# Performance work log

Measured on AMD Instinct MI355X. Metric: run time of the kernel, lower is better.

The kernel has to match this reference:

```python
import jax, jax.numpy as jnp
import numpy as np

N_DIS = 25000   # disease nodes: indices [0, 25000)
N_MIR = 25000   # mirna nodes:  indices [25000, 50000)
N = N_DIS + N_MIR
E = 600000
EMB = 128
HID = 128


def setup_inputs() -> dict:
    key = jax.random.key(0)
    ks = jax.random.split(key, 14)
    d_features = jax.random.normal(ks[0], (N_DIS, 383), jnp.float32)
    m_features = jax.random.normal(ks[1], (N_MIR, 495), jnp.float32)
    src = jax.random.randint(ks[2], (E,), 0, N, jnp.int32)
    dst = jax.random.randint(ks[3], (E,), 0, N, jnp.int32)
    def lin(k, fan_in, fan_out):
        lim = 1.0 / np.sqrt(fan_in)
        return jax.random.uniform(k, (fan_in, fan_out), jnp.float32, -lim, lim)
    return {
        "d_features": d_features,
        "m_features": m_features,
        "src": src,
        "dst": dst,
        "W_d": lin(ks[4], 383, EMB), "b_d": jnp.zeros((EMB,), jnp.float32),
        "W_m": lin(ks[5], 495, EMB), "b_m": jnp.zeros((EMB,), jnp.float32),
        "W_self1": lin(ks[6], EMB, HID), "W_neigh1": lin(ks[7], EMB, HID),
        "b1": jnp.zeros((HID,), jnp.float32),
        "W_self2": lin(ks[8], HID, HID), "W_neigh2": lin(ks[9], HID, HID),
        "b2": jnp.zeros((HID,), jnp.float32),
    }


def reference(d_features, m_features, src, dst,
              W_d, b_d, W_m, b_m,
              W_self1, W_neigh1, b1, W_self2, W_neigh2, b2):
    # Per-type embedding projection (torch.no_grad in original; dropout eval=identity)
    h_d = d_features @ W_d + b_d            # [N_DIS, EMB]
    h_m = m_features @ W_m + b_m            # [N_MIR, EMB]
    h = jnp.concatenate([h_d, h_m], axis=0)  # [N, EMB]

    # in-degree for mean aggregation (isolated nodes -> mean 0, like DGL fn.mean)
    deg = jax.ops.segment_sum(jnp.ones(src.shape, h.dtype), dst, num_segments=N)
    inv_deg = 1.0 / jnp.maximum(deg, 1.0)    # [N]

    def sage(x, W_self, W_neigh, b):
        # gather src feats, segment-mean into dst, then combine (DGL SAGEConv 'mean')
        agg = jax.ops.segment_sum(x[src], dst, num_segments=N) * inv_deg[:, None]
        return x @ W_self + agg @ W_neigh + b

    h = jax.nn.relu(sage(h, W_self1, W_neigh1, b1))
    h = sage(h, W_self2, W_neigh2, b2)
    return h
```

## Files before the change

### kernel.cpp

```cpp
#include <hip/hip_runtime.h>

#define N_DIS 25000
#define N_MIR 25000
#define NN    50000
#define E_NUM 600000
#define EMB   128

typedef __attribute__((ext_vector_type(8))) short short8v;
typedef __attribute__((ext_vector_type(4))) float floatx4;

typedef const unsigned int __attribute__((address_space(1))) as1_u32;
typedef unsigned int __attribute__((address_space(3))) as3_u32;

__device__ __forceinline__ void gld16(const void* g, void* lds) {
    __builtin_amdgcn_global_load_lds((as1_u32*)g, (as3_u32*)lds, 16, 0, 0);
}

__device__ __forceinline__ floatx4 mfma_bf16_16x16x32(short8v a, short8v b, floatx4 c) {
    asm("v_mfma_f32_16x16x32_bf16 %0, %1, %2, %0" : "+v"(c) : "v"(a), "v"(b));
    return c;
}

__device__ __forceinline__ float us2f(unsigned short u) {
    return __uint_as_float(((unsigned)u) << 16);
}
__device__ __forceinline__ unsigned short f2us(float f) {
    unsigned u = __float_as_uint(f);
    unsigned r = ((u >> 16) & 1u) + 0x7FFFu;
    u += r;
    return (unsigned short)(u >> 16);
}
__device__ __forceinline__ float loadf(const void* p, size_t i, bool isbf) {
    if (isbf) return us2f(((const unsigned short*)p)[i]);
    return ((const float*)p)[i];
}

__global__ __launch_bounds__(256) void gs_zero(int* counts, int* flags) {
    int i = blockIdx.x * blockDim.x + threadIdx.x;
    if (i < NN) counts[i] = 0;
    if (i < 8) flags[i] = 0;
}

__global__ __launch_bounds__(64) void gs_setflag(int* flags, int v) {
    if (threadIdx.x == 0) flags[0] = v;
}

__global__ __launch_bounds__(256) void gs_probe(const void* x, int* flags) {
    const unsigned* u = (const unsigned*)x;
    unsigned w = u[threadIdx.x];
    int e = (int)((w >> 7) & 0xFF);
    if (e >= 118 && e <= 135) atomicAdd(&flags[0], 1);
}

__global__ __launch_bounds__(256) void gs_prepw(const void* Wd, const void* Wm,
                                                const void* Ws1, const void* Wn1,
                                                const void* Ws2, const void* Wn2,
                                                const int* flags, unsigned short* wt) {
    const bool isbf = flags[0] > 128;
    const int t = threadIdx.x;
    const int w = blockIdx.x >> 2;
    const int cq = (blockIdx.x & 3) * 32;
    const void* W;
    unsigned short* oh;
    unsigned short* ol;
    int K, Kp;
    if (w == 0)      { W = Wd;  oh = wt + 0;      ol = wt + 49152;  K = 383; Kp = 384; }
    else if (w == 1) { W = Wm;  oh = wt + 98304;  ol = wt + 163840; K = 495; Kp = 512; }
    else if (w == 2) { W = Ws1; oh = wt + 229376; ol = wt + 245760; K = 128; Kp = 128; }
    else if (w == 3) { W = Wn1; oh = wt + 262144; ol = wt + 278528; K = 128; Kp = 128; }
    else if (w == 4) { W = Ws2; oh = wt + 294912; ol = wt + 311296; K = 128; Kp = 128; }
    else             { W = Wn2; oh = wt + 327680; ol = wt + 344064; K = 128; Kp = 128; }
    for (int c = cq; c < cq + 32; ++c) {
        for (int k = t; k < Kp; k += 256) {
            float x = (k < K) ? loadf(W, (size_t)k * EMB + c, isbf) : 0.f;
            unsigned short h = f2us(x);
            oh[(size_t)c * Kp + k] = h;
            ol[(size_t)c * Kp + k] = f2us(x - us2f(h));
        }
    }
}

__global__ __launch_bounds__(256) void gs_count(const int* dst, int* counts) {
    int e = blockIdx.x * blockDim.x + threadIdx.x;
    if (e < E_NUM) {
        unsigned d = (unsigned)dst[e];
        if (d < (unsigned)NN) atomicAdd(&counts[d], 1);
    }
}

__global__ __launch_bounds__(256) void gs_scan1(const int* counts, int* row_start, int* bsums) {
    __shared__ int tsum[256];
    const int t = threadIdx.x;
    const int base = blockIdx.x * 1024 + t * 4;
    int v0 = (base + 0 < NN) ? counts[base + 0] : 0;
    int v1 = (base + 1 < NN) ? counts[base + 1] : 0;
    int v2 = (base + 2 < NN) ? counts[base + 2] : 0;
    int v3 = (base + 3 < NN) ? counts[base + 3] : 0;
    int s = v0 + v1 + v2 + v3;
    tsum[t] = s;
    __syncthreads();
    for (int off = 1; off < 256; off <<= 1) {
        int xv = 0;
        if (t >= off) xv = tsum[t - off];
        __syncthreads();
        tsum[t] += xv;
        __syncthreads();
    }
    int excl = tsum[t] - s;
    if (base + 0 < NN) row_start[base + 0] = excl;
    excl += v0;
    if (base + 1 < NN) row_start[base + 1] = excl;
    excl += v1;
    if (base + 2 < NN) row_start[base + 2] = excl;
    excl += v2;
    if (base + 3 < NN) row_start[base + 3] = excl;
    if (t == 255) bsums[blockIdx.x] = tsum[255];
}

__global__ __launch_bounds__(64) void gs_scan2(int* bsums, int* row_start, int nb) {
    if (threadIdx.x == 0) {
        int run = 0;
        for (int i = 0; i < nb; ++i) {
            int v = bsums[i];
            bsums[i] = run;
            run += v;
        }
        row_start[NN] = run;
    }
}

__global__ __launch_bounds__(256) void gs_scan3(int* row_start, int* cursor, const int* bsums) {
    const int t = threadIdx.x;
    const int base = blockIdx.x * 1024 + t * 4;
    const int add = bsums[blockIdx.x];
    for (int i = 0; i < 4; ++i) {
        int idx = base + i;
        if (idx < NN) {
            int v = row_start[idx] + add;
            row_start[idx] = v;
            cursor[idx] = v;
        }
    }
}

__global__ __launch_bounds__(256) void gs_scatter(const int* src, const int* dst, int* cursor,
                                                  int* eidx) {
    int e = blockIdx.x * blockDim.x + threadIdx.x;
    if (e < E_NUM) {
        unsigned d = (unsigned)dst[e];
        unsigned sv = (unsigned)src[e];
        if (d < (unsigned)NN && sv < (unsigned)NN) {
            int p = atomicAdd(&cursor[d], 1);
            eidx[p] = (int)sv;
        }
    }
}

__global__ __launch_bounds__(256) void gs_aggp(const unsigned short* __restrict__ xh,
                                               const unsigned short* __restrict__ xl,
                                               const int* __restrict__ row_start,
                                               const int* __restrict__ eidx,
                                               unsigned short* __restrict__ oh,
                                               unsigned short* __restrict__ ol) {
    const int t = threadIdx.x;
    const int row = blockIdx.x * 8 + (t >> 5);
    const int c4 = (t & 31) * 4;
    if (row >= NN) return;
    const int s0 = row_start[row];
    const int s1 = row_start[row + 1];
    float a0 = 0.f, a1 = 0.f, a2 = 0.f, a3 = 0.f;
    float b0 = 0.f, b1 = 0.f, b2 = 0.f, b3 = 0.f;
    int e = s0;
    for (; e + 1 < s1; e += 2) {
        int sa = eidx[e];
        int sb = eidx[e + 1];
        ushort4 ha = *(const ushort4*)&xh[(size_t)sa * EMB + c4];
        ushort4 la = *(const ushort4*)&xl[(size_t)sa * EMB + c4];
        ushort4 hb = *(const ushort4*)&xh[(size_t)sb * EMB + c4];
        ushort4 lb = *(const ushort4*)&xl[(size_t)sb * EMB + c4];
        a0 += us2f(ha.x) + us2f(la.x); a1 += us2f(ha.y) + us2f(la.y);
        a2 += us2f(ha.z) + us2f(la.z); a3 += us2f(ha.w) + us2f(la.w);
        b0 += us2f(hb.x) + us2f(lb.x); b1 += us2f(hb.y) + us2f(lb.y);
        b2 += us2f(hb.z) + us2f(lb.z); b3 += us2f(hb.w) + us2f(lb.w);
    }
    if (e < s1) {
        int sa = eidx[e];
        ushort4 ha = *(const ushort4*)&xh[(size_t)sa * EMB + c4];
        ushort4 la = *(const ushort4*)&xl[(size_t)sa * EMB + c4];
        a0 += us2f(ha.x) + us2f(la.x); a1 += us2f(ha.y) + us2f(la.y);
        a2 += us2f(ha.z) + us2f(la.z); a3 += us2f(ha.w) + us2f(la.w);
    }
    float inv = (s1 > s0) ? 1.f / (float)(s1 - s0) : 0.f;
    float f0 = (a0 + b0) * inv, f1 = (a1 + b1) * inv;
    float f2 = (a2 + b2) * inv, f3 = (a3 + b3) * inv;
    ushort4 vh, vl;
    unsigned short h;
    h = f2us(f0); vh.x = h; vl.x = f2us(f0 - us2f(h));
    h = f2us(f1); vh.y = h; vl.y = f2us(f1 - us2f(h));
    h = f2us(f2); vh.z = h; vl.z = f2us(f2 - us2f(h));
    h = f2us(f3); vh.w = h; vl.w = f2us(f3 - us2f(h));
    *(ushort4*)&oh[(size_t)row * EMB + c4] = vh;
    *(ushort4*)&ol[(size_t)row * EMB + c4] = vl;
}

__global__ __launch_bounds__(256, 3) void gs_mmp(
    const void* __restrict__ Xa, int Ka, const unsigned short* __restrict__ WAh,
    const unsigned short* __restrict__ WAl, int KpA, const void* __restrict__ ba,
    const void* __restrict__ Xb, int Kb, const unsigned short* __restrict__ WBh,
    const unsigned short* __restrict__ WBl, int KpB, const void* __restrict__ bb,
    int splitB, int Ma, int Mb,
    const int* __restrict__ flags, unsigned short* __restrict__ outH,
    unsigned short* __restrict__ outL) {
    __shared__ __align__(16) unsigned char sm[49152];
    unsigned char* smXH = sm;
    unsigned char* smXL = sm + 8192;
    unsigned char* smWH = sm + 16384;
    unsigned char* smWL = sm + 32768;
    const bool isbf = flags[0] > 128;
    const int t = threadIdx.x;
    const bool sideB = (int)blockIdx.x >= splitB;
    const void* X1 = sideB ? Xb : Xa;
    const unsigned short* W1h = sideB ? WBh : WAh;
    const unsigned short* W1l = sideB ? WBl : WAl;
    const int K1 = sideB ? Kb : Ka;
    const int Kp1 = sideB ? KpB : KpA;
    const void* bias = sideB ? bb : ba;
    const int M = sideB ? Mb : Ma;
    const int r0 = (sideB ? ((int)blockIdx.x - splitB) : (int)blockIdx.x) * 64;
    unsigned short* oh = outH + (sideB ? (size_t)Ma * EMB : 0);
    unsigned short* ol = outL + (sideB ? (size_t)Ma * EMB : 0);

    const int l = t & 63;
    const int wv = t >> 6;
    const int wr = wv >> 1, wc = wv & 1;
    const int lr = l & 15, lg = l >> 4;

    floatx4 acc[2][4];
#pragma unroll
    for (int rt = 0; rt < 2; ++rt)
#pragma unroll
        for (int ct = 0; ct < 4; ++ct) acc[rt][ct] = (floatx4){0.f, 0.f, 0.f, 0.f};

    const int nch1 = (K1 + 63) >> 6;
    const int srX = t >> 2;
    const int skX = (t & 3) << 4;
    const bool xbf = isbf;

    for (int ch = 0; ch < nch1; ++ch) {
        const int ck0 = ch << 6;
        __syncthreads();
#pragma unroll
        for (int i = 0; i < 4; ++i) {
            const int p = (wv << 12) + (i << 10) + (l << 4);
            const int col = p >> 7;
            const int g16 = p & 0x7F;
            const size_t so = ((size_t)col * Kp1 + ck0) * 2 + (size_t)(g16 ^ ((col & 7) << 4));
            gld16((const unsigned char*)W1h + so, smWH + (wv << 12) + (i << 10));
            if (!isbf) gld16((const unsigned char*)W1l + so, smWL + (wv << 12) + (i << 10));
        }
        {
            const int gr = r0 + srX;
            unsigned xu[16];
#pragma unroll
            for (int j = 0; j < 16; ++j) {
                int gk = ck0 + skX + j;
                unsigned v = 0u;
                if (gr < M && gk < K1)
                    v = xbf ? (unsigned)((const unsigned short*)X1)[(size_t)gr * K1 + gk]
                            : ((const unsigned*)X1)[(size_t)gr * K1 + gk];
                xu[j] = v;
            }
            const int rowoff = srX << 7;
            const int swz = (srX & 7) << 4;
#pragma unroll
            for (int g = 0; g < 2; ++g) {
                short8v vh, vl;
#pragma unroll
                for (int e = 0; e < 8; ++e) {
                    unsigned u = xu[(g << 3) + e];
                    if (xbf) {
                        vh[e] = (short)u;
                        vl[e] = 0;
                    } else {
                        unsigned short h = (unsigned short)(u >> 16);
                        vh[e] = (short)h;
                        vl[e] = (short)f2us(__uint_as_float(u) - us2f(h));
                    }
                }
                const int off = rowoff + ((((skX << 1) + (g << 4))) ^ swz);
                *(short8v*)(smXH + off) = vh;
                if (!xbf) *(short8v*)(smXL + off) = vl;
            }
        }
        __syncthreads();
#pragma unroll
        for (int ks = 0; ks < 2; ++ks) {
            const int kbyte = (ks << 6) + (lg << 4);
            short8v ah[2], al[2];
#pragma unroll
            for (int rt = 0; rt < 2; ++rt) {
                const int row = wr * 32 + rt * 16 + lr;
                const int off = (row << 7) + (kbyte ^ ((row & 7) << 4));
                ah[rt] = *(const short8v*)(smXH + off);
                if (!xbf) al[rt] = *(const short8v*)(smXL + off);
            }
#pragma unroll
            for (int ct = 0; ct < 4; ++ct) {
                const int col = wc * 64 + ct * 16 + lr;
                const int boff = (col << 7) + (kbyte ^ ((col & 7) << 4));
                short8v bh = *(const short8v*)(smWH + boff);
                acc[0][ct] = mfma_bf16_16x16x32(ah[0], bh, acc[0][ct]);
                acc[1][ct] = mfma_bf16_16x16x32(ah[1], bh, acc[1][ct]);
                if (!xbf) {
                    acc[0][ct] = mfma_bf16_16x16x32(al[0], bh, acc[0][ct]);
                    acc[1][ct] = mfma_bf16_16x16x32(al[1], bh, acc[1][ct]);
                }
                if (!isbf) {
                    short8v bl = *(const short8v*)(smWL + boff);
                    acc[0][ct] = mfma_bf16_16x16x32(ah[0], bl, acc[0][ct]);
                    acc[1][ct] = mfma_bf16_16x16x32(ah[1], bl, acc[1][ct]);
                }
            }
        }
    }

#pragma unroll
    for (int ct = 0; ct < 4; ++ct) {
        const int col = wc * 64 + ct * 16 + lr;
        const float bbv = loadf(bias, col, isbf);
#pragma unroll
        for (int rt = 0; rt < 2; ++rt) {
#pragma unroll
            for (int rr = 0; rr < 4; ++rr) {
                const int row = r0 + wr * 32 + rt * 16 + (lg << 2) + rr;
                if (row < M) {
                    float v = acc[rt][ct][rr] + bbv;
                    unsigned short h = f2us(v);
                    oh[(size_t)row * EMB + col] = h;
                    ol[(size_t)row * EMB + col] = f2us(v - us2f(h));
                }
            }
        }
    }
}

__global__ __launch_bounds__(512, 4) void gs_mml(
    const unsigned short* __restrict__ X1h, const unsigned short* __restrict__ X1l,
    const unsigned short* __restrict__ W1h, const unsigned short* __restrict__ W1l,
    const unsigned short* __restrict__ X2h, const unsigned short* __restrict__ X2l,
    const unsigned short* __restrict__ W2h, const unsigned short* __restrict__ W2l,
    const void* __restrict__ bias, const int* __restrict__ flags,
    float* __restrict__ outf, unsigned short* __restrict__ outh,
    unsigned short* __restrict__ outl, int do_relu) {
    __shared__ __align__(16) unsigned char sm[65536];
    unsigned char* smXH = sm;
    unsigned char* smXL = sm + 16384;
    unsigned char* smWH = sm + 32768;
    unsigned char* smWL = sm + 49152;
    const bool isbf = flags[0] > 128;
    const int t = threadIdx.x;
    const int r0 = (int)blockIdx.x * 128;
    const int l = t & 63;
    const int wv = t >> 6;
    const int wr = wv >> 1, wc = wv & 1;
    const int lr = l & 15, lg = l >> 4;

    floatx4 acc[2][4];
#pragma unroll
    for (int rt = 0; rt < 2; ++rt)
#pragma unroll
        for (int ct = 0; ct < 4; ++ct) acc[rt][ct] = (floatx4){0.f, 0.f, 0.f, 0.f};

    const int plane = wv >> 1;

    for (int ch = 0; ch < 4; ++ch) {
        const unsigned short* xh = (ch < 2) ? X1h : X2h;
        const unsigned short* xl = (ch < 2) ? X1l : X2l;
        const unsigned short* wh = (ch < 2) ? W1h : W2h;
        const unsigned short* wl = (ch < 2) ? W1l : W2l;
        const int ck0b = (ch & 1) << 7;

        __syncthreads();
#pragma unroll
        for (int i = 0; i < 8; ++i) {
            const int q = ((wv & 1) << 13) + (i << 10) + (l << 4);
            const int rc = q >> 7;
            const int g16 = q & 0x7F;
            const int off = g16 ^ ((rc & 7) << 4);
            if (plane == 0) {
                const int gr = (r0 + rc < NN) ? (r0 + rc) : (NN - 1);
                gld16((const unsigned char*)xh + (size_t)gr * 256 + ck0b + off, smXH + q);
            } else if (plane == 1) {
                const int gr = (r0 + rc < NN) ? (r0 + rc) : (NN - 1);
                gld16((const unsigned char*)xl + (size_t)gr * 256 + ck0b + off, smXL + q);
            } else if (plane == 2) {
                gld16((const unsigned char*)wh + (size_t)rc * 256 + ck0b + off, smWH + q);
            } else if (!isbf) {
                gld16((const unsigned char*)wl + (size_t)rc * 256 + ck0b + off, smWL + q);
            }
        }
        __syncthreads();

#pragma unroll
        for (int ks = 0; ks < 2; ++ks) {
            const int kbyte = (ks << 6) + (lg << 4);
            short8v ah[2], al[2];
#pragma unroll
            for (int rt = 0; rt < 2; ++rt) {
                const int row = wr * 32 + rt * 16 + lr;
                const int off = (row << 7) + (kbyte ^ ((row & 7) << 4));
                ah[rt] = *(const short8v*)(smXH + off);
                al[rt] = *(const short8v*)(smXL + off);
            }
#pragma unroll
            for (int ct = 0; ct < 4; ++ct) {
                const int col = wc * 64 + ct * 16 + lr;
                const int boff = (col << 7) + (kbyte ^ ((col & 7) << 4));
                short8v bh = *(const short8v*)(smWH + boff);
                acc[0][ct] = mfma_bf16_16x16x32(ah[0], bh, acc[0][ct]);
                acc[1][ct] = mfma_bf16_16x16x32(ah[1], bh, acc[1][ct]);
                acc[0][ct] = mfma_bf16_16x16x32(al[0], bh, acc[0][ct]);
                acc[1][ct] = mfma_bf16_16x16x32(al[1], bh, acc[1][ct]);
                if (!isbf) {
                    short8v bl = *(const short8v*)(smWL + boff);
                    acc[0][ct] = mfma_bf16_16x16x32(ah[0], bl, acc[0][ct]);
                    acc[1][ct] = mfma_bf16_16x16x32(ah[1], bl, acc[1][ct]);
                }
            }
        }
    }

#pragma unroll
    for (int ct = 0; ct < 4; ++ct) {
        const int col = wc * 64 + ct * 16 + lr;
        const float bbv = loadf(bias, col, isbf);
#pragma unroll
        for (int rt = 0; rt < 2; ++rt) {
#pragma unroll
            for (int rr = 0; rr < 4; ++rr) {
                const int row = r0 + wr * 32 + rt * 16 + (lg << 2) + rr;
                if (row < NN) {
                    float v = acc[rt][ct][rr] + bbv;
                    if (do_relu) v = v > 0.f ? v : 0.f;
                    if (outf) {
                        outf[(size_t)row * EMB + col] = v;
                    } else {
                        unsigned short h = f2us(v);
                        outh[(size_t)row * EMB + col] = h;
                        outl[(size_t)row * EMB + col] = f2us(v - us2f(h));
                    }
                }
            }
        }
    }
}

extern "C" __attribute__((visibility("default"))) void kernel_launch(
    void* const* d_in, const int* in_sizes, int n_in, void* d_out, int out_size, void* d_ws,
    size_t ws_size, hipStream_t stream) {
    int iDF = 0, iMF = 1, iSRC = 2, iDST = 3, iWD = 4, iBD = 5, iWM = 6, iBM = 7;
    int iWS1 = 8, iWN1 = 9, iB1 = 10, iWS2 = 11, iWN2 = 12, iB2 = 13;
    long u0 = in_sizes ? (long)in_sizes[0] : 9575000L;
    int dt = -1;
    if (u0 == 49024L || u0 == 98048L || u0 == 196096L) {
        iWD = 0; iWM = 1; iWN1 = 2; iWN2 = 3; iWS1 = 4; iWS2 = 5;
        iB1 = 6; iB2 = 7; iBD = 8; iBM = 9; iDF = 10; iDST = 11; iMF = 12; iSRC = 13;
        if (u0 == 98048L) dt = 1;
        else if (u0 == 196096L) dt = 0;
    } else {
        if (u0 == 19150000L) dt = 1;
        else if (u0 == 38300000L) dt = 0;
    }
    const void* d_features = d_in[iDF];
    const void* m_features = d_in[iMF];
    const int* src = (const int*)d_in[iSRC];
    const int* dst = (const int*)d_in[iDST];
    const void* W_d = d_in[iWD];
    const void* b_d = d_in[iBD];
    const void* W_m = d_in[iWM];
    const void* b_m = d_in[iBM];
    const void* W_self1 = d_in[iWS1];
    const void* W_neigh1 = d_in[iWN1];
    const void* b1 = d_in[iB1];
    const void* W_self2 = d_in[iWS2];
    const void* W_neigh2 = d_in[iWN2];
    const void* b2v = d_in[iB2];

    char* w = (char*)d_ws;
    int* flags = (int*)(w + 0);
    int* counts = (int*)(w + 64);
    int* row_start = (int*)(w + 200064);
    int* cursor = (int*)(w + 400128);
    int* bsums = (int*)(w + 600128);
    int* eidx = (int*)(w + 600384);
    unsigned short* wt = (unsigned short*)(w + 3000448);
    unsigned short* wt_hd = wt + 0;
    unsigned short* wt_ld = wt + 49152;
    unsigned short* wt_hm = wt + 98304;
    unsigned short* wt_lm = wt + 163840;
    unsigned short* wt_hs1 = wt + 229376;
    unsigned short* wt_ls1 = wt + 245760;
    unsigned short* wt_hn1 = wt + 262144;
    unsigned short* wt_ln1 = wt + 278528;
    unsigned short* wt_hs2 = wt + 294912;
    unsigned short* wt_ls2 = wt + 311296;
    unsigned short* wt_hn2 = wt + 327680;
    unsigned short* wt_ln2 = wt + 344064;
    unsigned short* hFh = (unsigned short*)(w + 3721344);
    unsigned short* hFl = (unsigned short*)(w + 16521344);
    unsigned short* h1Fh = (unsigned short*)(w + 29321344);
    unsigned short* h1Fl = (unsigned short*)(w + 42121344);
    unsigned short* ag1h = (unsigned short*)d_out;
    unsigned short* ag1l = ag1h + 6400000;
    unsigned short* ag2h = hFh;
    unsigned short* ag2l = hFl;

    const int NB_SCAN = (NN + 1023) / 1024;
    const int EB = (E_NUM + 255) / 256;
    const int ZB = (NN + 255) / 256;

    hipLaunchKernelGGL(gs_zero, dim3(ZB), dim3(256), 0, stream, counts, flags);
    if (dt == 1)
        hipLaunchKernelGGL(gs_setflag, dim3(1), dim3(64), 0, stream, flags, 1000);
    else if (dt == 0)
        hipLaunchKernelGGL(gs_setflag, dim3(1), dim3(64), 0, stream, flags, 0);
    else
        hipLaunchKernelGGL(gs_probe, dim3(1), dim3(256), 0, stream, d_features, flags);

    hipLaunchKernelGGL(gs_prepw, dim3(24), dim3(256), 0, stream, W_d, W_m, W_self1, W_neigh1,
                       W_self2, W_neigh2, flags, wt);

    hipLaunchKernelGGL(gs_count, dim3(EB), dim3(256), 0, stream, dst, counts);
    hipLaunchKernelGGL(gs_scan1, dim3(NB_SCAN), dim3(256), 0, stream, counts, row_start, bsums);
    hipLaunchKernelGGL(gs_scan2, dim3(1), dim3(64), 0, stream, bsums, row_start, NB_SCAN);
    hipLaunchKernelGGL(gs_scan3, dim3(NB_SCAN), dim3(256), 0, stream, row_start, cursor, bsums);
    hipLaunchKernelGGL(gs_scatter, dim3(EB), dim3(256), 0, stream, src, dst, cursor, eidx);

    const int PBd = (N_DIS + 63) / 64;
    hipLaunchKernelGGL(gs_mmp, dim3(2 * PBd), dim3(256), 0, stream,
                       d_features, 383, wt_hd, wt_ld, 384, b_d,
                       m_features, 495, wt_hm, wt_lm, 512, b_m,
                       PBd, N_DIS, N_MIR, flags, hFh, hFl);

    const int AB = NN / 8;
    const int GBL = (NN + 127) / 128;

    hipLaunchKernelGGL(gs_aggp, dim3(AB), dim3(256), 0, stream, hFh, hFl, row_start, eidx,
                       ag1h, ag1l);
    hipLaunchKernelGGL(gs_mml, dim3(GBL), dim3(512), 0, stream,
                       hFh, hFl, wt_hs1, wt_ls1, ag1h, ag1l, wt_hn1, wt_ln1,
                       b1, flags, (float*)nullptr, h1Fh, h1Fl, 1);

    hipLaunchKernelGGL(gs_aggp, dim3(AB), dim3(256), 0, stream, h1Fh, h1Fl, row_start, eidx,
                       ag2h, ag2l);
    hipLaunchKernelGGL(gs_mml, dim3(GBL), dim3(512), 0, stream,
                       h1Fh, h1Fl, wt_hs2, wt_ls2, ag2h, ag2l, wt_hn2, wt_ln2,
                       b2v, flags, (float*)d_out, (unsigned short*)nullptr,
                       (unsigned short*)nullptr, 0);
}
```

Measured before the change: 434.8 us.

## Double-buffer LDS staging in projection and SAGE GEMMs with smaller K chunks

Both GEMM kernels (input projection and SAGE combine) now use a two-buffer LDS pipeline. The loads for the next K-chunk are issued before the MFMA work on the current chunk, and the second barrier per chunk is dropped. K chunks shrink to 32, and the hi/lo planes of X and W are interleaved inside one 128-byte row per buffer. gs_mml also moves from 128-row/512-thread blocks to 64-row/256-thread blocks to fit the doubled buffers and raise block count. The aim is to hide global-load latency, at the cost of more loop iterations, more barriers in total and more register pressure.

```diff
diff --git a/kernel.cpp b/kernel.cpp
--- a/kernel.cpp
+++ b/kernel.cpp
@@ -203,6 +203,7 @@
     *(ushort4*)&ol[(size_t)row * EMB + c4] = vl;
 }
 
+
 __global__ __launch_bounds__(256, 3) void gs_mmp(
     const void* __restrict__ Xa, int Ka, const unsigned short* __restrict__ WAh,
     const unsigned short* __restrict__ WAl, int KpA, const void* __restrict__ ba,
@@ -212,10 +213,6 @@
     const int* __restrict__ flags, unsigned short* __restrict__ outH,
     unsigned short* __restrict__ outL) {
     __shared__ __align__(16) unsigned char sm[49152];
-    unsigned char* smXH = sm;
-    unsigned char* smXL = sm + 8192;
-    unsigned char* smWH = sm + 16384;
-    unsigned char* smWL = sm + 32768;
     const bool isbf = flags[0] > 128;
     const int t = threadIdx.x;
     const bool sideB = (int)blockIdx.x >= splitB;
@@ -229,6 +226,7 @@
     const int r0 = (sideB ? ((int)blockIdx.x - splitB) : (int)blockIdx.x) * 64;
     unsigned short* oh = outH + (sideB ? (size_t)Ma * EMB : 0);
     unsigned short* ol = outL + (sideB ? (size_t)Ma * EMB : 0);
+    const bool xbf = isbf;
 
     const int l = t & 63;
     const int wv = t >> 6;
@@ -241,87 +239,106 @@
 #pragma unroll
         for (int ct = 0; ct < 4; ++ct) acc[rt][ct] = (floatx4){0.f, 0.f, 0.f, 0.f};
 
-    const int nch1 = (K1 + 63) >> 6;
+    const int nch = (K1 + 31) >> 5;
+
     const int srX = t >> 2;
-    const int skX = (t & 3) << 4;
-    const bool xbf = isbf;
-
-    for (int ch = 0; ch < nch1; ++ch) {
-        const int ck0 = ch << 6;
+    const int k8 = (t & 3) << 3;
+    const int xoff_h = srX * 128 + ((((t & 3)) ^ (srX & 7)) << 4);
+    int wdst[4], wlo[4];
+    size_t wso[4];
+#pragma unroll
+    for (int i = 0; i < 4; ++i) {
+        const int p = (i * 256 + t) << 4;
+        const int col = p >> 7;
+        const int g = ((p >> 4) & 7) ^ (col & 7);
+        wlo[i] = g >> 2;
+        wso[i] = (size_t)col * ((size_t)Kp1 << 1) + (size_t)((g & 3) << 4);
+        wdst[i] = 8192 + p;
+    }
+
+    unsigned xu[8];
+    auto XLOAD = [&](int ck0) {
+        const int gr = r0 + srX;
+#pragma unroll
+        for (int j = 0; j < 8; ++j) {
+            const int gk = ck0 + k8 + j;
+            unsigned v = 0u;
+            if (gr < M && gk < K1)
+                v = xbf ? (unsigned)((const unsigned short*)X1)[(size_t)gr * K1 + gk]
+                        : ((const unsigned*)X1)[(size_t)gr * K1 + gk];
+            xu[j] = v;
+        }
+    };
+    auto WSTAGE = [&](int buf, int ck0) {
+        const size_t kb = (size_t)ck0 << 1;
+        unsigned char* bb_ = sm + buf * 24576;
+#pragma unroll
+        for (int i = 0; i < 4; ++i) {
+            const unsigned char* srcb =
+                wlo[i] ? (const unsigned char*)W1l : (const unsigned char*)W1h;
+            gld16(srcb + wso[i] + kb, bb_ + wdst[i]);
+        }
+    };
+    auto XWRITE = [&](int buf) {
+        short8v vh, vl;
+#pragma unroll
+        for (int e = 0; e < 8; ++e) {
+            const unsigned u = xu[e];
+            if (xbf) {
+                vh[e] = (short)u;
+                vl[e] = 0;
+            } else {
+                const unsigned short h = (unsigned short)(u >> 16);
+                vh[e] = (short)h;
+                vl[e] = (short)f2us(__uint_as_float(u) - us2f(h));
+            }
+        }
+        unsigned char* bb_ = sm + buf * 24576;
+        *(short8v*)(bb_ + xoff_h) = vh;
+        *(short8v*)(bb_ + (xoff_h ^ 64)) = vl;
+    };
+    auto COMPUTE = [&](int buf) {
+        unsigned char* bb_ = sm + buf * 24576;
+        short8v ah[2], al[2];
+#pragma unroll
+        for (int rt = 0; rt < 2; ++rt) {
+            const int row = wr * 32 + rt * 16 + lr;
+            const int aoff = row * 128 + ((lg ^ (row & 7)) << 4);
+            ah[rt] = *(const short8v*)(bb_ + aoff);
+            if (!xbf) al[rt] = *(const short8v*)(bb_ + (aoff ^ 64));
+        }
+#pragma unroll
+        for (int ct = 0; ct < 4; ++ct) {
+            const int col = wc * 64 + ct * 16 + lr;
+            const int boff = 8192 + col * 128 + ((lg ^ (col & 7)) << 4);
+            short8v bh = *(const short8v*)(bb_ + boff);
+            acc[0][ct] = mfma_bf16_16x16x32(ah[0], bh, acc[0][ct]);
+            acc[1][ct] = mfma_bf16_16x16x32(ah[1], bh, acc[1][ct]);
+            if (!xbf) {
+                acc[0][ct] = mfma_bf16_16x16x32(al[0], bh, acc[0][ct]);
+                acc[1][ct] = mfma_bf16_16x16x32(al[1], bh, acc[1][ct]);
+            }
+            if (!isbf) {
+                short8v bl = *(const short8v*)(bb_ + (boff ^ 64));
+                acc[0][ct] = mfma_bf16_16x16x32(ah[0], bl, acc[0][ct]);
+                acc[1][ct] = mfma_bf16_16x16x32(ah[1], bl, acc[1][ct]);
+            }
+        }
+    };
+
+    XLOAD(0);
+    WSTAGE(0, 0);
+    XWRITE(0);
+    int cur = 0;
+    for (int ch = 0; ch < nch; ++ch) {
         __syncthreads();
-#pragma unroll
-        for (int i = 0; i < 4; ++i) {
-            const int p = (wv << 12) + (i << 10) + (l << 4);
-            const int col = p >> 7;
-            const int g16 = p & 0x7F;
-            const size_t so = ((size_t)col * Kp1 + ck0) * 2 + (size_t)(g16 ^ ((col & 7) << 4));
-            gld16((const unsigned char*)W1h + so, smWH + (wv << 12) + (i << 10));
-            if (!isbf) gld16((const unsigned char*)W1l + so, smWL + (wv << 12) + (i << 10));
-        }
-        {
-            const int gr = r0 + srX;
-            unsigned xu[16];
-#pragma unroll
-            for (int j = 0; j < 16; ++j) {
-                int gk = ck0 + skX + j;
-                unsigned v = 0u;
-                if (gr < M && gk < K1)
-                    v = xbf ? (unsigned)((const unsigned short*)X1)[(size_t)gr * K1 + gk]
-                            : ((const unsigned*)X1)[(size_t)gr * K1 + gk];
-                xu[j] = v;
-            }
-            const int rowoff = srX << 7;
-            const int swz = (srX & 7) << 4;
-#pragma unroll
-            for (int g = 0; g < 2; ++g) {
-                short8v vh, vl;
-#pragma unroll
-                for (int e = 0; e < 8; ++e) {
-                    unsigned u = xu[(g << 3) + e];
-                    if (xbf) {
-                        vh[e] = (short)u;
-                        vl[e] = 0;
-                    } else {
-                        unsigned short h = (unsigned short)(u >> 16);
-                        vh[e] = (short)h;
-                        vl[e] = (short)f2us(__uint_as_float(u) - us2f(h));
-                    }
-                }
-                const int off = rowoff + ((((skX << 1) + (g << 4))) ^ swz);
-                *(short8v*)(smXH + off) = vh;
-                if (!xbf) *(short8v*)(smXL + off) = vl;
-            }
-        }
-        __syncthreads();
-#pragma unroll
-        for (int ks = 0; ks < 2; ++ks) {
-            const int kbyte = (ks << 6) + (lg << 4);
-            short8v ah[2], al[2];
-#pragma unroll
-            for (int rt = 0; rt < 2; ++rt) {
-                const int row = wr * 32 + rt * 16 + lr;
-                const int off = (row << 7) + (kbyte ^ ((row & 7) << 4));
-                ah[rt] = *(const short8v*)(smXH + off);
-                if (!xbf) al[rt] = *(const short8v*)(smXL + off);
-            }
-#pragma unroll
-            for (int ct = 0; ct < 4; ++ct) {
-                const int col = wc * 64 + ct * 16 + lr;
-                const int boff = (col << 7) + (kbyte ^ ((col & 7) << 4));
-                short8v bh = *(const short8v*)(smWH + boff);
-                acc[0][ct] = mfma_bf16_16x16x32(ah[0], bh, acc[0][ct]);
-                acc[1][ct] = mfma_bf16_16x16x32(ah[1], bh, acc[1][ct]);
-                if (!xbf) {
-                    acc[0][ct] = mfma_bf16_16x16x32(al[0], bh, acc[0][ct]);
-                    acc[1][ct] = mfma_bf16_16x16x32(al[1], bh, acc[1][ct]);
-                }
-                if (!isbf) {
-                    short8v bl = *(const short8v*)(smWL + boff);
-                    acc[0][ct] = mfma_bf16_16x16x32(ah[0], bl, acc[0][ct]);
-                    acc[1][ct] = mfma_bf16_16x16x32(ah[1], bl, acc[1][ct]);
-                }
-            }
-        }
+        if (ch + 1 < nch) {
+            XLOAD((ch + 1) << 5);
+            WSTAGE(cur ^ 1, (ch + 1) << 5);
+        }
+        COMPUTE(cur);
+        if (ch + 1 < nch) XWRITE(cur ^ 1);
+        cur ^= 1;
     }
 
 #pragma unroll
@@ -334,8 +351,8 @@
             for (int rr = 0; rr < 4; ++rr) {
                 const int row = r0 + wr * 32 + rt * 16 + (lg << 2) + rr;
                 if (row < M) {
-                    float v = acc[rt][ct][rr] + bbv;
-                    unsigned short h = f2us(v);
+                    const float v = acc[rt][ct][rr] + bbv;
+                    const unsigned short h = f2us(v);
                     oh[(size_t)row * EMB + col] = h;
                     ol[(size_t)row * EMB + col] = f2us(v - us2f(h));
                 }
@@ -344,7 +361,7 @@
     }
 }
 
-__global__ __launch_bounds__(512, 4) void gs_mml(
+__global__ __launch_bounds__(256, 3) void gs_mml(
     const unsigned short* __restrict__ X1h, const unsigned short* __restrict__ X1l,
     const unsigned short* __restrict__ W1h, const unsigned short* __restrict__ W1l,
     const unsigned short* __restrict__ X2h, const unsigned short* __restrict__ X2l,
@@ -352,14 +369,10 @@
     const void* __restrict__ bias, const int* __restrict__ flags,
     float* __restrict__ outf, unsigned short* __restrict__ outh,
     unsigned short* __restrict__ outl, int do_relu) {
-    __shared__ __align__(16) unsigned char sm[65536];
-    unsigned char* smXH = sm;
-    unsigned char* smXL = sm + 16384;
-    unsigned char* smWH = sm + 32768;
-    unsigned char* smWL = sm + 49152;
+    __shared__ __align__(16) unsigned char sm[49152];
     const bool isbf = flags[0] > 128;
     const int t = threadIdx.x;
-    const int r0 = (int)blockIdx.x * 128;
+    const int r0 = (int)blockIdx.x * 64;
     const int l = t & 63;
     const int wv = t >> 6;
     const int wr = wv >> 1, wc = wv & 1;
@@ -371,63 +384,72 @@
 #pragma unroll
         for (int ct = 0; ct < 4; ++ct) acc[rt][ct] = (floatx4){0.f, 0.f, 0.f, 0.f};
 
-    const int plane = wv >> 1;
-
-    for (int ch = 0; ch < 4; ++ch) {
-        const unsigned short* xh = (ch < 2) ? X1h : X2h;
-        const unsigned short* xl = (ch < 2) ? X1l : X2l;
-        const unsigned short* wh = (ch < 2) ? W1h : W2h;
-        const unsigned short* wl = (ch < 2) ? W1l : W2l;
-        const int ck0b = (ch & 1) << 7;
-
+    int sIsX[6], sLo[6], sDst[6];
+    size_t sOff[6];
+#pragma unroll
+    for (int i = 0; i < 6; ++i) {
+        const int idx = i * 256 + t;
+        const int isx = (idx < 512) ? 1 : 0;
+        const int p = (isx ? idx : (idx - 512)) << 4;
+        const int rc = p >> 7;
+        const int g = ((p >> 4) & 7) ^ (rc & 7);
+        sIsX[i] = isx;
+        sLo[i] = g >> 2;
+        const int gr = isx ? ((r0 + rc < NN) ? (r0 + rc) : (NN - 1)) : rc;
+        sOff[i] = (size_t)gr * 256 + (size_t)((g & 3) << 4);
+        sDst[i] = (isx ? 0 : 8192) + p;
+    }
+
+    auto STAGE = [&](int buf, int ch) {
+        const unsigned short* xh = (ch < 4) ? X1h : X2h;
+        const unsigned short* xl = (ch < 4) ? X1l : X2l;
+        const unsigned short* wh = (ch < 4) ? W1h : W2h;
+        const unsigned short* wl = (ch < 4) ? W1l : W2l;
+        const size_t kb = (size_t)(ch & 3) << 6;
+        unsigned char* bb_ = sm + buf * 24576;
+#pragma unroll
+        for (int i = 0; i < 6; ++i) {
+            const unsigned char* srcb =
+                sIsX[i] ? (sLo[i] ? (const unsigned char*)xl : (const unsigned char*)xh)
+                        : (sLo[i] ? (const unsigned char*)wl : (const unsigned char*)wh);
+            gld16(srcb + sOff[i] + kb, bb_ + sDst[i]);
+        }
+    };
+    auto COMPUTE = [&](int buf) {
+        unsigned char* bb_ = sm + buf * 24576;
+        short8v ah[2], al[2];
+#pragma unroll
+        for (int rt = 0; rt < 2; ++rt) {
+            const int row = wr * 32 + rt * 16 + lr;
+            const int aoff = row * 128 + ((lg ^ (row & 7)) << 4);
+            ah[rt] = *(const short8v*)(bb_ + aoff);
+            al[rt] = *(const short8v*)(bb_ + (aoff ^ 64));
+        }
+#pragma unroll
+        for (int ct = 0; ct < 4; ++ct) {
+            const int col = wc * 64 + ct * 16 + lr;
+            const int boff = 8192 + col * 128 + ((lg ^ (col & 7)) << 4);
+            short8v bh = *(const short8v*)(bb_ + boff);
+            acc[0][ct] = mfma_bf16_16x16x32(ah[0], bh, acc[0][ct]);
+            acc[1][ct] = mfma_bf16_16x16x32(ah[1], bh, acc[1][ct]);
+            acc[0][ct] = mfma_bf16_16x16x32(al[0], bh, acc[0][ct]);
+            acc[1][ct] = mfma_bf16_16x16x32(al[1], bh, acc[1][ct]);
+            if (!isbf) {
+                short8v bl = *(const short8v*)(bb_ + (boff ^ 64));
+                acc[0][ct] = mfma_bf16_16x16x32(ah[0], bl, acc[0][ct]);
+                acc[1][ct] = mfma_bf16_16x16x32(ah[1], bl, acc[1][ct]);
+            }
+        }
+    };
+
+    STAGE(0, 0);
+    int cur = 0;
+#pragma unroll
+    for (int ch = 0; ch < 8; ++ch) {
         __syncthreads();
-#pragma unroll
-        for (int i = 0; i < 8; ++i) {
-            const int q = ((wv & 1) << 13) + (i << 10) + (l << 4);
-            const int rc = q >> 7;
-            const int g16 = q & 0x7F;
-            const int off = g16 ^ ((rc & 7) << 4);
-            if (plane == 0) {
-                const int gr = (r0 + rc < NN) ? (r0 + rc) : (NN - 1);
-                gld16((const unsigned char*)xh + (size_t)gr * 256 + ck0b + off, smXH + q);
-            } else if (plane == 1) {
-                const int gr = (r0 + rc < NN) ? (r0 + rc) : (NN - 1);
-                gld16((const unsigned char*)xl + (size_t)gr * 256 + ck0b + off, smXL + q);
-            } else if (plane == 2) {
-                gld16((const unsigned char*)wh + (size_t)rc * 256 + ck0b + off, smWH + q);
-            } else if (!isbf) {
-                gld16((const unsigned char*)wl + (size_t)rc * 256 + ck0b + off, smWL + q);
-            }
-        }
-        __syncthreads();
-
-#pragma unroll
-        for (int ks = 0; ks < 2; ++ks) {
-            const int kbyte = (ks << 6) + (lg << 4);
-            short8v ah[2], al[2];
-#pragma unroll
-            for (int rt = 0; rt < 2; ++rt) {
-                const int row = wr * 32 + rt * 16 + lr;
-                const int off = (row << 7) + (kbyte ^ ((row & 7) << 4));
-                ah[rt] = *(const short8v*)(smXH + off);
-                al[rt] = *(const short8v*)(smXL + off);
-            }
-#pragma unroll
-            for (int ct = 0; ct < 4; ++ct) {
-                const int col = wc * 64 + ct * 16 + lr;
-                const int boff = (col << 7) + (kbyte ^ ((col & 7) << 4));
-                short8v bh = *(const short8v*)(smWH + boff);
-                acc[0][ct] = mfma_bf16_16x16x32(ah[0], bh, acc[0][ct]);
-                acc[1][ct] = mfma_bf16_16x16x32(ah[1], bh, acc[1][ct]);
-                acc[0][ct] = mfma_bf16_16x16x32(al[0], bh, acc[0][ct]);
-                acc[1][ct] = mfma_bf16_16x16x32(al[1], bh, acc[1][ct]);
-                if (!isbf) {
-                    short8v bl = *(const short8v*)(smWL + boff);
-                    acc[0][ct] = mfma_bf16_16x16x32(ah[0], bl, acc[0][ct]);
-                    acc[1][ct] = mfma_bf16_16x16x32(ah[1], bl, acc[1][ct]);
-                }
-            }
-        }
+        if (ch + 1 < 8) STAGE(cur ^ 1, ch + 1);
+        COMPUTE(cur);
+        cur ^= 1;
     }
 
 #pragma unroll
@@ -445,7 +467,7 @@
                     if (outf) {
                         outf[(size_t)row * EMB + col] = v;
                     } else {
-                        unsigned short h = f2us(v);
+                        const unsigned short h = f2us(v);
                         outh[(size_t)row * EMB + col] = h;
                         outl[(size_t)row * EMB + col] = f2us(v - us2f(h));
                     }
@@ -543,17 +565,17 @@
                        PBd, N_DIS, N_MIR, flags, hFh, hFl);
 
     const int AB = NN / 8;
-    const int GBL = (NN + 127) / 128;
+    const int GBL = (NN + 63) / 64;
 
     hipLaunchKernelGGL(gs_aggp, dim3(AB), dim3(256), 0, stream, hFh, hFl, row_start, eidx,
                        ag1h, ag1l);
-    hipLaunchKernelGGL(gs_mml, dim3(GBL), dim3(512), 0, stream,
+    hipLaunchKernelGGL(gs_mml, dim3(GBL), dim3(256), 0, stream,
                        hFh, hFl, wt_hs1, wt_ls1, ag1h, ag1l, wt_hn1, wt_ln1,
                        b1, flags, (float*)nullptr, h1Fh, h1Fl, 1);
 
     hipLaunchKernelGGL(gs_aggp, dim3(AB), dim3(256), 0, stream, h1Fh, h1Fl, row_start, eidx,
                        ag2h, ag2l);
-    hipLaunchKernelGGL(gs_mml, dim3(GBL), dim3(512), 0, stream,
+    hipLaunchKernelGGL(gs_mml, dim3(GBL), dim3(256), 0, stream,
                        h1Fh, h1Fl, wt_hs2, wt_ls2, ag2h, ag2l, wt_hn2, wt_ln2,
                        b2v, flags, (float*)d_out, (unsigned short*)nullptr,
                        (unsigned short*)nullptr, 0);
```

Result: slower. 455.1 us (+4.7%).
